# Optimization experiments

Measured on AMD Instinct MI355X. Metric: run time of the kernel, lower is better.

The kernel has to match this reference:

```python
import jax
jax.config.update("jax_enable_x64", True)
import jax.numpy as jnp
import numpy as np

SCALE = 1 << 16  # 65536 fixed-point scale
HALF = SCALE // 2

DIM = 4096
HIDDEN = 11008  # multiple_of * ceil(int(2*16384/3)/256)
TOKENS = 1024


def setup_inputs() -> dict:
    key = jax.random.key(0)
    kx, k1, k2, k3 = jax.random.split(key, 4)
    # Integer-valued fixed-point activations (torch code treats x as int32).
    x = jax.random.randint(kx, (TOKENS, DIM), 0, 256, dtype=jnp.int32)
    # Learned float weights (quantized to int32 fixed-point inside forward).
    w1 = jax.random.normal(k1, (HIDDEN, DIM), dtype=jnp.float32) * 0.02
    w2 = jax.random.normal(k2, (DIM, HIDDEN), dtype=jnp.float32) * 0.02
    w3 = jax.random.normal(k3, (HIDDEN, DIM), dtype=jnp.float32) * 0.02
    return {"x": x, "w1": w1, "w2": w2, "w3": w3}


def reference(x, w1, w2, w3):
    # Quantize weights to int32 fixed point (round half-to-even, like torch.round).
    w1i = jnp.round(w1.astype(jnp.float64) * SCALE).astype(jnp.int32)
    w2i = jnp.round(w2.astype(jnp.float64) * SCALE).astype(jnp.int32)
    w3i = jnp.round(w3.astype(jnp.float64) * SCALE).astype(jnp.int32)

    xf = x.astype(jnp.float64)  # [T, D]
    # Emulated integer GEMMs via fp64 matmul, truncated to int64 (exact here).
    t1 = jnp.matmul(xf, w1i.T.astype(jnp.float64)).astype(jnp.int64)  # [T, H]
    t3 = jnp.matmul(xf, w3i.T.astype(jnp.float64)).astype(jnp.int64)  # [T, H]

    # Requantize up-projection: rounding floor-div by SCALE (int floor division).
    q3 = ((t3 + HALF) // SCALE).astype(jnp.int32)

    # Gate path: requantize, dequantize to fp16, SiLU, re-quantize to int32.
    g = (t1 + HALF) // SCALE
    g = (g.astype(jnp.float64) / SCALE).astype(jnp.float16)
    g = jax.nn.silu(g)  # fp16 SiLU, matching F.silu on half
    g = jnp.round(g.astype(jnp.float64) * SCALE).astype(jnp.int32)

    # Fixed-point elementwise product with rounding requantization.
    t13 = ((g.astype(jnp.int64) * q3.astype(jnp.int64) + HALF) // SCALE).astype(jnp.int32)

    # Down projection GEMM + final requantization.
    t123 = jnp.matmul(t13.astype(jnp.float64), w2i.T.astype(jnp.float64)).astype(jnp.int64)
    out = ((t123 + HALF) // SCALE).astype(jnp.int32)  # [T, D]
    return out
```

## Files before the change

### kernel.cpp

```cpp
#include <hip/hip_runtime.h>
#include <hip/hip_fp16.h>
#include <math.h>

#define TOK  1024
#define DIMK 4096
#define HID  11008

typedef long long ll;
typedef int v4i  __attribute__((ext_vector_type(4)));
typedef int v16i __attribute__((ext_vector_type(16)));

#define T13_OFF 0ull
#define LUT_OFF 11272192ull
#define CS1_OFF (LUT_OFF + 32768ull)
#define CS3_OFF (CS1_OFF + 44032ull)
#define XQ_OFF  (CS3_OFF + 44032ull)
#define WQ_OFF  (XQ_OFF + 4194304ull)
#define PLANE   45088768ull
#define WS_NEED (WQ_OFF + 6ull * PLANE)

__device__ __forceinline__ int gate_requant(int g) {
  const float vf = __half2float(__float2half((float)g * (1.0f / 65536.0f)));
  const float e32 = (float)exp(-(double)vf);
  const float e16 = __half2float(__float2half(e32));
  const float d16 = __half2float(__float2half(1.0f + e16));
  const float s16 = __half2float(__float2half(1.0f / d16));
  const float p16 = __half2float(__float2half(vf * s16));
  return __float2int_rn(p16 * 65536.0f);
}

__device__ __forceinline__ v16i vzero16() {
  v16i z;
  #pragma unroll
  for (int i = 0; i < 16; ++i) z[i] = 0;
  return z;
}

__device__ __forceinline__ void gll(const void* g, void* l) {
  __builtin_amdgcn_global_load_lds((const __attribute__((address_space(1))) unsigned int*)g,
                                   (__attribute__((address_space(3))) unsigned int*)l,
                                   16, 0, 0);
}


__global__ void lut_kernel(int* __restrict__ lut) {
  const int i = blockIdx.x * blockDim.x + threadIdx.x;
  lut[i] = gate_requant(i - 4096);
}

__global__ __launch_bounds__(256)
void xq_kernel(const int* __restrict__ x, char* __restrict__ xq) {
  const size_t base = ((size_t)blockIdx.x * 256 + threadIdx.x) * 16;
  int w[4];
  #pragma unroll
  for (int i = 0; i < 4; ++i) {
    const int4 v = *reinterpret_cast<const int4*>(&x[base + i * 4]);
    w[i] = ((v.x & 255) | ((v.y & 255) << 8) | ((v.z & 255) << 16) | ((v.w & 255) << 24)) ^ 0x80808080;
  }
  *reinterpret_cast<int4*>(&xq[base]) = make_int4(w[0], w[1], w[2], w[3]);
}

__global__ __launch_bounds__(256)
void prequant_all(const float* __restrict__ w1, const float* __restrict__ w3,
                  const float* __restrict__ w2, char* __restrict__ wq,
                  int* __restrict__ cs1, int* __restrict__ cs3)
{
  const int bid = blockIdx.x;
  const int m = bid / 11008;
  const int rb = bid - m * 11008;
  const float* src = (m == 0) ? w1 : ((m == 1) ? w3 : w2);
  int4* lo = (int4*)(wq + (size_t)(2 * m) * PLANE);
  int4* hi = (int4*)(wq + (size_t)(2 * m + 1) * PLANE);
  const int t = threadIdx.x;
  const size_t fbase = (size_t)rb * 4096 + (size_t)t * 16;

  int sum = 0;
  int lob[4], hib[4];
  #pragma unroll
  for (int i = 0; i < 4; ++i) {
    const float4 f = *reinterpret_cast<const float4*>(&src[fbase + i * 4]);
    const int q0 = __float2int_rn(f.x * 65536.0f);
    const int q1 = __float2int_rn(f.y * 65536.0f);
    const int q2 = __float2int_rn(f.z * 65536.0f);
    const int q3 = __float2int_rn(f.w * 65536.0f);
    sum += q0 + q1 + q2 + q3;
    lob[i] = (q0 & 127) | ((q1 & 127) << 8) | ((q2 & 127) << 16) | ((q3 & 127) << 24);
    hib[i] = ((q0 >> 7) & 255) | (((q1 >> 7) & 255) << 8) |
             (((q2 >> 7) & 255) << 16) | (((q3 >> 7) & 255) << 24);
  }
  const size_t o = (size_t)rb * 256 + t;
  lo[o] = make_int4(lob[0], lob[1], lob[2], lob[3]);
  hi[o] = make_int4(hib[0], hib[1], hib[2], hib[3]);
  if (m < 2) {
    #pragma unroll
    for (int off = 32; off > 0; off >>= 1) sum += __shfl_xor(sum, off, 64);
    if ((t & 63) == 0) atomicAdd(((m == 0) ? cs1 : cs3) + rb, sum);
  }
}

#define UP_BUF 32768

__global__ __launch_bounds__(512, 1)
void up_gemm(const char* __restrict__ xq, const char* __restrict__ wq,
             const int* __restrict__ csum1, const int* __restrict__ csum3,
             const int* __restrict__ lut, char* __restrict__ t13)
{
  __shared__ char smem[3 * UP_BUF];
  const int tid = threadIdx.x;
  const int w = tid >> 6, l = tid & 63;
  const int rf = w & 3, cf = w >> 2;
  const int l16 = l * 16;

  const int flat = blockIdx.x;
  const int g = (flat & 7) * 86 + (flat >> 3);
  const int col0 = (g >> 2) * 64;
  const int row0 = (g & 3) * 256;

  const char* gA = xq + (size_t)(row0 + w * 32 + (l & 31)) * DIMK + (l >> 5) * 16;
  const char* gB = wq + (size_t)(w >> 1) * PLANE
                 + (size_t)(col0 + (w & 1) * 32 + (l & 31)) * DIMK + (l >> 5) * 16;
  const unsigned dA0 = (2 * w + 0) * 1024, dA1 = (2 * w + 1) * 1024;
  const unsigned dB0 = 16384 + (2 * w + 0) * 1024, dB1 = 16384 + (2 * w + 1) * 1024;

  v16i acc[2][4];
  #pragma unroll
  for (int m = 0; m < 2; ++m)
    #pragma unroll
    for (int p = 0; p < 4; ++p) acc[m][p] = vzero16();

  gll(gA, smem + dA0);       gll(gA + 32, smem + dA1);
  gll(gB, smem + dB0);       gll(gB + 32, smem + dB1);
  gll(gA + 64, smem + UP_BUF + dA0);  gll(gA + 96, smem + UP_BUF + dA1);
  gll(gB + 64, smem + UP_BUF + dB0);  gll(gB + 96, smem + UP_BUF + dB1);
  asm volatile("s_waitcnt vmcnt(4)" ::: "memory");
  __builtin_amdgcn_s_barrier();

  const int NT = DIMK / 64;
  unsigned co = 0, so = 2 * UP_BUF;
  for (int kt = 0; kt < NT; ++kt) {
    const char* sb = smem + co;
    const bool st = (kt + 2 < NT);
    const int kb = (kt + 2) * 64;
    {
      const v4i av0 = *(const v4i*)(sb + (rf * 4 + 0) * 1024 + l16);
      const v4i av1 = *(const v4i*)(sb + (rf * 4 + 2) * 1024 + l16);
      const v4i b0  = *(const v4i*)(sb + 16384 + (0 * 4 + cf * 2) * 1024 + l16);
      const v4i b1  = *(const v4i*)(sb + 16384 + (1 * 4 + cf * 2) * 1024 + l16);
      const v4i b2  = *(const v4i*)(sb + 16384 + (2 * 4 + cf * 2) * 1024 + l16);
      const v4i b3  = *(const v4i*)(sb + 16384 + (3 * 4 + cf * 2) * 1024 + l16);
      if (st) { gll(gA + kb, smem + so + dA0); gll(gA + kb + 32, smem + so + dA1); }
      __builtin_amdgcn_s_barrier();
      asm volatile("s_waitcnt lgkmcnt(0)" ::: "memory");
      __builtin_amdgcn_sched_barrier(0);
      __builtin_amdgcn_s_setprio(1);
      acc[0][0] = __builtin_amdgcn_mfma_i32_32x32x32_i8(av0, b0, acc[0][0], 0, 0, 0);
      acc[0][1] = __builtin_amdgcn_mfma_i32_32x32x32_i8(av0, b1, acc[0][1], 0, 0, 0);
      acc[0][2] = __builtin_amdgcn_mfma_i32_32x32x32_i8(av0, b2, acc[0][2], 0, 0, 0);
      acc[0][3] = __builtin_amdgcn_mfma_i32_32x32x32_i8(av0, b3, acc[0][3], 0, 0, 0);
      acc[1][0] = __builtin_amdgcn_mfma_i32_32x32x32_i8(av1, b0, acc[1][0], 0, 0, 0);
      acc[1][1] = __builtin_amdgcn_mfma_i32_32x32x32_i8(av1, b1, acc[1][1], 0, 0, 0);
      acc[1][2] = __builtin_amdgcn_mfma_i32_32x32x32_i8(av1, b2, acc[1][2], 0, 0, 0);
      acc[1][3] = __builtin_amdgcn_mfma_i32_32x32x32_i8(av1, b3, acc[1][3], 0, 0, 0);
      __builtin_amdgcn_s_setprio(0);
      __builtin_amdgcn_s_barrier();
    }
    {
      const v4i av0 = *(const v4i*)(sb + (rf * 4 + 1) * 1024 + l16);
      const v4i av1 = *(const v4i*)(sb + (rf * 4 + 3) * 1024 + l16);
      const v4i b0  = *(const v4i*)(sb + 16384 + (0 * 4 + cf * 2 + 1) * 1024 + l16);
      const v4i b1  = *(const v4i*)(sb + 16384 + (1 * 4 + cf * 2 + 1) * 1024 + l16);
      const v4i b2  = *(const v4i*)(sb + 16384 + (2 * 4 + cf * 2 + 1) * 1024 + l16);
      const v4i b3  = *(const v4i*)(sb + 16384 + (3 * 4 + cf * 2 + 1) * 1024 + l16);
      if (st) { gll(gB + kb, smem + so + dB0); gll(gB + kb + 32, smem + so + dB1); }
      __builtin_amdgcn_s_barrier();
      asm volatile("s_waitcnt lgkmcnt(0)" ::: "memory");
      __builtin_amdgcn_sched_barrier(0);
      __builtin_amdgcn_s_setprio(1);
      acc[0][0] = __builtin_amdgcn_mfma_i32_32x32x32_i8(av0, b0, acc[0][0], 0, 0, 0);
      acc[0][1] = __builtin_amdgcn_mfma_i32_32x32x32_i8(av0, b1, acc[0][1], 0, 0, 0);
      acc[0][2] = __builtin_amdgcn_mfma_i32_32x32x32_i8(av0, b2, acc[0][2], 0, 0, 0);
      acc[0][3] = __builtin_amdgcn_mfma_i32_32x32x32_i8(av0, b3, acc[0][3], 0, 0, 0);
      acc[1][0] = __builtin_amdgcn_mfma_i32_32x32x32_i8(av1, b0, acc[1][0], 0, 0, 0);
      acc[1][1] = __builtin_amdgcn_mfma_i32_32x32x32_i8(av1, b1, acc[1][1], 0, 0, 0);
      acc[1][2] = __builtin_amdgcn_mfma_i32_32x32x32_i8(av1, b2, acc[1][2], 0, 0, 0);
      acc[1][3] = __builtin_amdgcn_mfma_i32_32x32x32_i8(av1, b3, acc[1][3], 0, 0, 0);
      __builtin_amdgcn_s_setprio(0);
      if (st) { asm volatile("s_waitcnt vmcnt(4)" ::: "memory"); }
      else    { asm volatile("s_waitcnt vmcnt(0)" ::: "memory"); }
      __builtin_amdgcn_s_barrier();
    }
    if (st) so = (so == 2 * UP_BUF) ? 0 : so + UP_BUF;
    co = (co == 2 * UP_BUF) ? 0 : co + UP_BUF;
  }

  const int col = col0 + cf * 32 + (l & 31);
  const int cs1v = csum1[col], cs3v = csum3[col];
  #pragma unroll
  for (int m = 0; m < 2; ++m) {
    #pragma unroll
    for (int r = 0; r < 16; ++r) {
      const int row = row0 + rf * 64 + m * 32 + (r & 3) + 8 * (r >> 2) + 4 * (l >> 5);
      const ll t1 = (ll)acc[m][0][r] + (((ll)acc[m][1][r] + cs1v) << 7);
      int gg = (int)((t1 + 32768) >> 16);
      gg = gg < -4096 ? -4096 : (gg > 4095 ? 4095 : gg);
      const ll t3 = (ll)acc[m][2][r] + (((ll)acc[m][3][r] + cs3v) << 7);
      const int q3 = (int)((t3 + 32768) >> 16);
      const int gate = lut[gg + 4096];
      t13[(size_t)row * HID + col] = (char)((int)(((ll)gate * q3 + 32768) >> 16));
    }
  }
}

#define DN_BUF 24576

__global__ __launch_bounds__(512, 1)
void down_gemm(const char* __restrict__ t13, const char* __restrict__ w2lo,
               const char* __restrict__ w2hi, int* __restrict__ out)
{
  __shared__ char smem[3 * DN_BUF];
  const int tid = threadIdx.x;
  const int w = tid >> 6, l = tid & 63;
  const int rf = w & 3, cf = w >> 2;
  const int l16 = l * 16;

  const int flat = blockIdx.x;
  const int g = (flat & 7) * 32 + (flat >> 3);
  const int col0 = (g >> 2) * 64;
  const int row0 = (g & 3) * 256;

  const char* gA = t13 + (size_t)(row0 + w * 32 + (l & 31)) * HID + (l >> 5) * 16;
  const char* pB = (w >> 2) ? w2hi : w2lo;
  const char* gB = pB + (size_t)(col0 + ((w >> 1) & 1) * 32 + (l & 31)) * HID
                 + (w & 1) * 32 + (l >> 5) * 16;
  const unsigned dA0 = (2 * w + 0) * 1024, dA1 = (2 * w + 1) * 1024;
  const unsigned dB = 16384 + w * 1024;

  v16i acc[2][2];
  #pragma unroll
  for (int m = 0; m < 2; ++m)
    #pragma unroll
    for (int p = 0; p < 2; ++p) acc[m][p] = vzero16();

  gll(gA, smem + dA0);  gll(gA + 32, smem + dA1);  gll(gB, smem + dB);
  gll(gA + 64, smem + DN_BUF + dA0);  gll(gA + 96, smem + DN_BUF + dA1);
  gll(gB + 64, smem + DN_BUF + dB);
  asm volatile("s_waitcnt vmcnt(3)" ::: "memory");
  __builtin_amdgcn_s_barrier();

  const int NT = HID / 64;
  unsigned co = 0, so = 2 * DN_BUF;
  for (int kt = 0; kt < NT; ++kt) {
    const char* sb = smem + co;
    const bool st = (kt + 2 < NT);
    const int kb = (kt + 2) * 64;
    {
      const v4i av0 = *(const v4i*)(sb + (rf * 4 + 0) * 1024 + l16);
      const v4i av1 = *(const v4i*)(sb + (rf * 4 + 2) * 1024 + l16);
      const v4i bL  = *(const v4i*)(sb + 16384 + (0 * 4 + cf * 2) * 1024 + l16);
      const v4i bH  = *(const v4i*)(sb + 16384 + (1 * 4 + cf * 2) * 1024 + l16);
      if (st) { gll(gA + kb, smem + so + dA0); gll(gA + kb + 32, smem + so + dA1); }
      __builtin_amdgcn_s_barrier();
      asm volatile("s_waitcnt lgkmcnt(0)" ::: "memory");
      __builtin_amdgcn_sched_barrier(0);
      __builtin_amdgcn_s_setprio(1);
      acc[0][0] = __builtin_amdgcn_mfma_i32_32x32x32_i8(av0, bL, acc[0][0], 0, 0, 0);
      acc[0][1] = __builtin_amdgcn_mfma_i32_32x32x32_i8(av0, bH, acc[0][1], 0, 0, 0);
      acc[1][0] = __builtin_amdgcn_mfma_i32_32x32x32_i8(av1, bL, acc[1][0], 0, 0, 0);
      acc[1][1] = __builtin_amdgcn_mfma_i32_32x32x32_i8(av1, bH, acc[1][1], 0, 0, 0);
      __builtin_amdgcn_s_setprio(0);
      __builtin_amdgcn_s_barrier();
    }
    {
      const v4i av0 = *(const v4i*)(sb + (rf * 4 + 1) * 1024 + l16);
      const v4i av1 = *(const v4i*)(sb + (rf * 4 + 3) * 1024 + l16);
      const v4i bL  = *(const v4i*)(sb + 16384 + (0 * 4 + cf * 2 + 1) * 1024 + l16);
      const v4i bH  = *(const v4i*)(sb + 16384 + (1 * 4 + cf * 2 + 1) * 1024 + l16);
      if (st) { gll(gB + kb, smem + so + dB); }
      __builtin_amdgcn_s_barrier();
      asm volatile("s_waitcnt lgkmcnt(0)" ::: "memory");
      __builtin_amdgcn_sched_barrier(0);
      __builtin_amdgcn_s_setprio(1);
      acc[0][0] = __builtin_amdgcn_mfma_i32_32x32x32_i8(av0, bL, acc[0][0], 0, 0, 0);
      acc[0][1] = __builtin_amdgcn_mfma_i32_32x32x32_i8(av0, bH, acc[0][1], 0, 0, 0);
      acc[1][0] = __builtin_amdgcn_mfma_i32_32x32x32_i8(av1, bL, acc[1][0], 0, 0, 0);
      acc[1][1] = __builtin_amdgcn_mfma_i32_32x32x32_i8(av1, bH, acc[1][1], 0, 0, 0);
      __builtin_amdgcn_s_setprio(0);
      if (st) { asm volatile("s_waitcnt vmcnt(3)" ::: "memory"); }
      else    { asm volatile("s_waitcnt vmcnt(0)" ::: "memory"); }
      __builtin_amdgcn_s_barrier();
    }
    if (st) so = (so == 2 * DN_BUF) ? 0 : so + DN_BUF;
    co = (co == 2 * DN_BUF) ? 0 : co + DN_BUF;
  }

  const int col = col0 + cf * 32 + (l & 31);
  #pragma unroll
  for (int m = 0; m < 2; ++m) {
    #pragma unroll
    for (int r = 0; r < 16; ++r) {
      const int row = row0 + rf * 64 + m * 32 + (r & 3) + 8 * (r >> 2) + 4 * (l >> 5);
      out[(size_t)row * DIMK + col] =
          (int)((((ll)acc[m][0][r] + ((ll)acc[m][1][r] << 7)) + 32768) >> 16);
    }
  }
}

#define BT 64
#define BN 64
#define BK 64
#define LDST 68

__device__ __forceinline__ int mad24(int a, int b, int c) {
  return ((a << 8) >> 8) * ((b << 8) >> 8) + c;
}

__global__ __launch_bounds__(256)
void ffn_up_f(const int* __restrict__ x, const float* __restrict__ w1,
              const float* __restrict__ w3, short* __restrict__ t13)
{
  __shared__ int As[BT][LDST];
  __shared__ int B1[BK][LDST];
  __shared__ int B3[BK][LDST];
  const int tx = threadIdx.x, ty = threadIdx.y;
  const int tid = ty * 16 + tx;
  const int col0 = blockIdx.x * BN;
  const int row0 = blockIdx.y * BT;
  const int lr = tid >> 4;
  const int lk = (tid & 15) << 2;
  int acc1[16] = {0};
  int acc3[16] = {0};
  for (int k0 = 0; k0 < DIMK; k0 += BK) {
    #pragma unroll
    for (int m = 0; m < 4; ++m) {
      const int r = lr + m * 16;
      *reinterpret_cast<int4*>(&As[r][lk]) =
          *reinterpret_cast<const int4*>(&x[(size_t)(row0 + r) * DIMK + k0 + lk]);
      const float4 f1 = *reinterpret_cast<const float4*>(&w1[(size_t)(col0 + r) * DIMK + k0 + lk]);
      const float4 f3 = *reinterpret_cast<const float4*>(&w3[(size_t)(col0 + r) * DIMK + k0 + lk]);
      B1[lk + 0][r] = __float2int_rn(f1.x * 65536.0f);
      B1[lk + 1][r] = __float2int_rn(f1.y * 65536.0f);
      B1[lk + 2][r] = __float2int_rn(f1.z * 65536.0f);
      B1[lk + 3][r] = __float2int_rn(f1.w * 65536.0f);
      B3[lk + 0][r] = __float2int_rn(f3.x * 65536.0f);
      B3[lk + 1][r] = __float2int_rn(f3.y * 65536.0f);
      B3[lk + 2][r] = __float2int_rn(f3.z * 65536.0f);
      B3[lk + 3][r] = __float2int_rn(f3.w * 65536.0f);
    }
    __syncthreads();
    #pragma unroll 8
    for (int kk = 0; kk < BK; ++kk) {
      const int4 b1 = *reinterpret_cast<const int4*>(&B1[kk][tx << 2]);
      const int4 b3 = *reinterpret_cast<const int4*>(&B3[kk][tx << 2]);
      #pragma unroll
      for (int i = 0; i < 4; ++i) {
        const int av = As[(ty << 2) + i][kk] & 255;
        acc1[i*4+0] = mad24(av, b1.x, acc1[i*4+0]);
        acc1[i*4+1] = mad24(av, b1.y, acc1[i*4+1]);
        acc1[i*4+2] = mad24(av, b1.z, acc1[i*4+2]);
        acc1[i*4+3] = mad24(av, b1.w, acc1[i*4+3]);
        acc3[i*4+0] = mad24(av, b3.x, acc3[i*4+0]);
        acc3[i*4+1] = mad24(av, b3.y, acc3[i*4+1]);
        acc3[i*4+2] = mad24(av, b3.z, acc3[i*4+2]);
        acc3[i*4+3] = mad24(av, b3.w, acc3[i*4+3]);
      }
    }
    __syncthreads();
  }
  #pragma unroll
  for (int i = 0; i < 4; ++i) {
    #pragma unroll
    for (int j = 0; j < 4; ++j) {
      const int g    = (acc1[i*4+j] + 32768) >> 16;
      const int q3   = (acc3[i*4+j] + 32768) >> 16;
      const int gate = gate_requant(g);
      const int tv = (int)(((ll)gate * (ll)q3 + 32768) >> 16);
      t13[(size_t)(row0 + (ty<<2) + i) * HID + col0 + (tx<<2) + j] = (short)tv;
    }
  }
}

__global__ __launch_bounds__(256)
void ffn_down_f(const short* __restrict__ t13, const float* __restrict__ w2,
                int* __restrict__ out)
{
  __shared__ int As[BT][LDST];
  __shared__ int Bs[BK][LDST];
  const int tx = threadIdx.x, ty = threadIdx.y;
  const int tid = ty * 16 + tx;
  const int col0 = blockIdx.x * BN;
  const int row0 = blockIdx.y * BT;
  const int lr = tid >> 4;
  const int lk = (tid & 15) << 2;
  const int ar = tid >> 3;
  const int ak = (tid & 7) << 3;
  int acc[16] = {0};
  for (int k0 = 0; k0 < HID; k0 += BK) {
    #pragma unroll
    for (int m = 0; m < 2; ++m) {
      const int r = ar + m * 32;
      const int4 v = *reinterpret_cast<const int4*>(&t13[(size_t)(row0 + r) * HID + k0 + ak]);
      As[r][ak+0] = (v.x << 16) >> 16;  As[r][ak+1] = v.x >> 16;
      As[r][ak+2] = (v.y << 16) >> 16;  As[r][ak+3] = v.y >> 16;
      As[r][ak+4] = (v.z << 16) >> 16;  As[r][ak+5] = v.z >> 16;
      As[r][ak+6] = (v.w << 16) >> 16;  As[r][ak+7] = v.w >> 16;
    }
    #pragma unroll
    for (int m = 0; m < 4; ++m) {
      const int r = lr + m * 16;
      const float4 f = *reinterpret_cast<const float4*>(&w2[(size_t)(col0 + r) * HID + k0 + lk]);
      Bs[lk + 0][r] = __float2int_rn(f.x * 65536.0f);
      Bs[lk + 1][r] = __float2int_rn(f.y * 65536.0f);
      Bs[lk + 2][r] = __float2int_rn(f.z * 65536.0f);
      Bs[lk + 3][r] = __float2int_rn(f.w * 65536.0f);
    }
    __syncthreads();
    #pragma unroll 8
    for (int kk = 0; kk < BK; ++kk) {
      const int4 b = *reinterpret_cast<const int4*>(&Bs[kk][tx << 2]);
      #pragma unroll
      for (int i = 0; i < 4; ++i) {
        const int av = As[(ty << 2) + i][kk];
        acc[i*4+0] = mad24(av, b.x, acc[i*4+0]);
        acc[i*4+1] = mad24(av, b.y, acc[i*4+1]);
        acc[i*4+2] = mad24(av, b.z, acc[i*4+2]);
        acc[i*4+3] = mad24(av, b.w, acc[i*4+3]);
      }
    }
    __syncthreads();
  }
  #pragma unroll
  for (int i = 0; i < 4; ++i) {
    #pragma unroll
    for (int j = 0; j < 4; ++j) {
      out[(size_t)(row0 + (ty<<2) + i) * DIMK + col0 + (tx<<2) + j] =
          (acc[i*4+j] + 32768) >> 16;
    }
  }
}

extern "C" void kernel_launch(void* const* d_in, const int* in_sizes, int n_in,
                              void* d_out, int out_size, void* d_ws, size_t ws_size,
                              hipStream_t stream) {
  (void)in_sizes; (void)n_in; (void)out_size;
  const int*   x  = (const int*)d_in[0];
  const float* w1 = (const float*)d_in[1];
  const float* w2 = (const float*)d_in[2];
  const float* w3 = (const float*)d_in[3];
  int* out = (int*)d_out;
  char* ws = (char*)d_ws;

  if (ws_size >= WS_NEED) {
    char* t13 = ws + T13_OFF;
    int*  lut = (int*)(ws + LUT_OFF);
    int*  cs1 = (int*)(ws + CS1_OFF);
    int*  cs3 = (int*)(ws + CS3_OFF);
    char* xq  = ws + XQ_OFF;
    char* wq  = ws + WQ_OFF;

    hipMemsetAsync(ws + CS1_OFF, 0, 88064, stream);
    hipLaunchKernelGGL(lut_kernel, dim3(32), dim3(256), 0, stream, lut);
    hipLaunchKernelGGL(xq_kernel, dim3(1024), dim3(256), 0, stream, x, xq);
    hipLaunchKernelGGL(prequant_all, dim3(33024), dim3(256), 0, stream,
                       w1, w3, w2, wq, cs1, cs3);
    hipLaunchKernelGGL(up_gemm, dim3(688), dim3(512), 0, stream,
                       xq, wq, cs1, cs3, lut, t13);
    hipLaunchKernelGGL(down_gemm, dim3(256), dim3(512), 0, stream,
                       t13, wq + 4 * PLANE, wq + 5 * PLANE, out);
  } else {
    if (ws_size < (size_t)TOK * HID * sizeof(short)) return;
    short* t13 = (short*)ws;
    dim3 blk(16, 16);
    hipLaunchKernelGGL(ffn_up_f,   dim3(HID / BN, TOK / BT), blk, 0, stream, x, w1, w3, t13);
    hipLaunchKernelGGL(ffn_down_f, dim3(DIMK / BN, TOK / BT), blk, 0, stream, t13, w2, out);
  }
}
```

Measured before the change: 513.4 us.

## Replace LDS-staged up GEMM with direct global-to-register double-buffered loads

The up-projection GEMM no longer stages A and B tiles through a triple-buffered LDS ring with barriers. Each wave now loads its own MFMA operands straight from global memory into registers, double-buffered across k-steps, and launch bounds are raised to allow two blocks per CU. This removes LDS traffic and barrier synchronisation, but every wave now re-fetches data that was previously shared across waves. That multiplies global and L2 traffic for the shared A rows and B columns and raises register pressure.

```diff
diff --git a/kernel.cpp b/kernel.cpp
--- a/kernel.cpp
+++ b/kernel.cpp
@@ -98,29 +98,28 @@
   }
 }
 
-#define UP_BUF 32768
-
-__global__ __launch_bounds__(512, 1)
+
+__global__ __launch_bounds__(512, 2)
 void up_gemm(const char* __restrict__ xq, const char* __restrict__ wq,
              const int* __restrict__ csum1, const int* __restrict__ csum3,
              const int* __restrict__ lut, char* __restrict__ t13)
 {
-  __shared__ char smem[3 * UP_BUF];
   const int tid = threadIdx.x;
   const int w = tid >> 6, l = tid & 63;
   const int rf = w & 3, cf = w >> 2;
-  const int l16 = l * 16;
 
   const int flat = blockIdx.x;
   const int g = (flat & 7) * 86 + (flat >> 3);
   const int col0 = (g >> 2) * 64;
   const int row0 = (g & 3) * 256;
 
-  const char* gA = xq + (size_t)(row0 + w * 32 + (l & 31)) * DIMK + (l >> 5) * 16;
-  const char* gB = wq + (size_t)(w >> 1) * PLANE
-                 + (size_t)(col0 + (w & 1) * 32 + (l & 31)) * DIMK + (l >> 5) * 16;
-  const unsigned dA0 = (2 * w + 0) * 1024, dA1 = (2 * w + 1) * 1024;
-  const unsigned dB0 = 16384 + (2 * w + 0) * 1024, dB1 = 16384 + (2 * w + 1) * 1024;
+  const char* pa0 = xq + (size_t)(row0 + rf * 64 +  0 + (l & 31)) * DIMK + (l >> 5) * 16;
+  const char* pa1 = xq + (size_t)(row0 + rf * 64 + 32 + (l & 31)) * DIMK + (l >> 5) * 16;
+  const size_t offB = (size_t)(col0 + cf * 32 + (l & 31)) * DIMK + (l >> 5) * 16;
+  const char* pb0 = wq + 0ull * PLANE + offB;
+  const char* pb1 = wq + 1ull * PLANE + offB;
+  const char* pb2 = wq + 2ull * PLANE + offB;
+  const char* pb3 = wq + 3ull * PLANE + offB;
 
   v16i acc[2][4];
   #pragma unroll
@@ -128,70 +127,38 @@
     #pragma unroll
     for (int p = 0; p < 4; ++p) acc[m][p] = vzero16();
 
-  gll(gA, smem + dA0);       gll(gA + 32, smem + dA1);
-  gll(gB, smem + dB0);       gll(gB + 32, smem + dB1);
-  gll(gA + 64, smem + UP_BUF + dA0);  gll(gA + 96, smem + UP_BUF + dA1);
-  gll(gB + 64, smem + UP_BUF + dB0);  gll(gB + 96, smem + UP_BUF + dB1);
-  asm volatile("s_waitcnt vmcnt(4)" ::: "memory");
-  __builtin_amdgcn_s_barrier();
+  v4i a0[2][2], b0[4][2];
+  v4i a1[2][2], b1[4][2];
+
+  #define UP_LOAD(A, B, kb) { \
+    A[0][0] = *(const v4i*)(pa0 + (kb));      A[0][1] = *(const v4i*)(pa0 + (kb) + 32); \
+    A[1][0] = *(const v4i*)(pa1 + (kb));      A[1][1] = *(const v4i*)(pa1 + (kb) + 32); \
+    B[0][0] = *(const v4i*)(pb0 + (kb));      B[0][1] = *(const v4i*)(pb0 + (kb) + 32); \
+    B[1][0] = *(const v4i*)(pb1 + (kb));      B[1][1] = *(const v4i*)(pb1 + (kb) + 32); \
+    B[2][0] = *(const v4i*)(pb2 + (kb));      B[2][1] = *(const v4i*)(pb2 + (kb) + 32); \
+    B[3][0] = *(const v4i*)(pb3 + (kb));      B[3][1] = *(const v4i*)(pb3 + (kb) + 32); }
+
+  #define UP_MFMA(A, B) { \
+    _Pragma("unroll") \
+    for (int ks = 0; ks < 2; ++ks) { \
+      _Pragma("unroll") \
+      for (int m = 0; m < 2; ++m) { \
+        _Pragma("unroll") \
+        for (int p = 0; p < 4; ++p) { \
+          acc[m][p] = __builtin_amdgcn_mfma_i32_32x32x32_i8(A[m][ks], B[p][ks], acc[m][p], 0, 0, 0); \
+        } } } }
 
   const int NT = DIMK / 64;
-  unsigned co = 0, so = 2 * UP_BUF;
-  for (int kt = 0; kt < NT; ++kt) {
-    const char* sb = smem + co;
-    const bool st = (kt + 2 < NT);
-    const int kb = (kt + 2) * 64;
-    {
-      const v4i av0 = *(const v4i*)(sb + (rf * 4 + 0) * 1024 + l16);
-      const v4i av1 = *(const v4i*)(sb + (rf * 4 + 2) * 1024 + l16);
-      const v4i b0  = *(const v4i*)(sb + 16384 + (0 * 4 + cf * 2) * 1024 + l16);
-      const v4i b1  = *(const v4i*)(sb + 16384 + (1 * 4 + cf * 2) * 1024 + l16);
-      const v4i b2  = *(const v4i*)(sb + 16384 + (2 * 4 + cf * 2) * 1024 + l16);
-      const v4i b3  = *(const v4i*)(sb + 16384 + (3 * 4 + cf * 2) * 1024 + l16);
-      if (st) { gll(gA + kb, smem + so + dA0); gll(gA + kb + 32, smem + so + dA1); }
-      __builtin_amdgcn_s_barrier();
-      asm volatile("s_waitcnt lgkmcnt(0)" ::: "memory");
-      __builtin_amdgcn_sched_barrier(0);
-      __builtin_amdgcn_s_setprio(1);
-      acc[0][0] = __builtin_amdgcn_mfma_i32_32x32x32_i8(av0, b0, acc[0][0], 0, 0, 0);
-      acc[0][1] = __builtin_amdgcn_mfma_i32_32x32x32_i8(av0, b1, acc[0][1], 0, 0, 0);
-      acc[0][2] = __builtin_amdgcn_mfma_i32_32x32x32_i8(av0, b2, acc[0][2], 0, 0, 0);
-      acc[0][3] = __builtin_amdgcn_mfma_i32_32x32x32_i8(av0, b3, acc[0][3], 0, 0, 0);
-      acc[1][0] = __builtin_amdgcn_mfma_i32_32x32x32_i8(av1, b0, acc[1][0], 0, 0, 0);
-      acc[1][1] = __builtin_amdgcn_mfma_i32_32x32x32_i8(av1, b1, acc[1][1], 0, 0, 0);
-      acc[1][2] = __builtin_amdgcn_mfma_i32_32x32x32_i8(av1, b2, acc[1][2], 0, 0, 0);
-      acc[1][3] = __builtin_amdgcn_mfma_i32_32x32x32_i8(av1, b3, acc[1][3], 0, 0, 0);
-      __builtin_amdgcn_s_setprio(0);
-      __builtin_amdgcn_s_barrier();
-    }
-    {
-      const v4i av0 = *(const v4i*)(sb + (rf * 4 + 1) * 1024 + l16);
-      const v4i av1 = *(const v4i*)(sb + (rf * 4 + 3) * 1024 + l16);
-      const v4i b0  = *(const v4i*)(sb + 16384 + (0 * 4 + cf * 2 + 1) * 1024 + l16);
-      const v4i b1  = *(const v4i*)(sb + 16384 + (1 * 4 + cf * 2 + 1) * 1024 + l16);
-      const v4i b2  = *(const v4i*)(sb + 16384 + (2 * 4 + cf * 2 + 1) * 1024 + l16);
-      const v4i b3  = *(const v4i*)(sb + 16384 + (3 * 4 + cf * 2 + 1) * 1024 + l16);
-      if (st) { gll(gB + kb, smem + so + dB0); gll(gB + kb + 32, smem + so + dB1); }
-      __builtin_amdgcn_s_barrier();
-      asm volatile("s_waitcnt lgkmcnt(0)" ::: "memory");
-      __builtin_amdgcn_sched_barrier(0);
-      __builtin_amdgcn_s_setprio(1);
-      acc[0][0] = __builtin_amdgcn_mfma_i32_32x32x32_i8(av0, b0, acc[0][0], 0, 0, 0);
-      acc[0][1] = __builtin_amdgcn_mfma_i32_32x32x32_i8(av0, b1, acc[0][1], 0, 0, 0);
-      acc[0][2] = __builtin_amdgcn_mfma_i32_32x32x32_i8(av0, b2, acc[0][2], 0, 0, 0);
-      acc[0][3] = __builtin_amdgcn_mfma_i32_32x32x32_i8(av0, b3, acc[0][3], 0, 0, 0);
-      acc[1][0] = __builtin_amdgcn_mfma_i32_32x32x32_i8(av1, b0, acc[1][0], 0, 0, 0);
-      acc[1][1] = __builtin_amdgcn_mfma_i32_32x32x32_i8(av1, b1, acc[1][1], 0, 0, 0);
-      acc[1][2] = __builtin_amdgcn_mfma_i32_32x32x32_i8(av1, b2, acc[1][2], 0, 0, 0);
-      acc[1][3] = __builtin_amdgcn_mfma_i32_32x32x32_i8(av1, b3, acc[1][3], 0, 0, 0);
-      __builtin_amdgcn_s_setprio(0);
-      if (st) { asm volatile("s_waitcnt vmcnt(4)" ::: "memory"); }
-      else    { asm volatile("s_waitcnt vmcnt(0)" ::: "memory"); }
-      __builtin_amdgcn_s_barrier();
-    }
-    if (st) so = (so == 2 * UP_BUF) ? 0 : so + UP_BUF;
-    co = (co == 2 * UP_BUF) ? 0 : co + UP_BUF;
-  }
+  UP_LOAD(a0, b0, 0)
+  #pragma unroll 1
+  for (int kt = 0; kt < NT; kt += 2) {
+    UP_LOAD(a1, b1, (kt + 1) * 64)
+    UP_MFMA(a0, b0)
+    if (kt + 2 < NT) { UP_LOAD(a0, b0, (kt + 2) * 64) }
+    UP_MFMA(a1, b1)
+  }
+  #undef UP_LOAD
+  #undef UP_MFMA
 
   const int col = col0 + cf * 32 + (l & 31);
   const int cs1v = csum1[col], cs3v = csum3[col];
```

Result: slower. 842.7 us (+64.1%).

## Overlap w2 prequantization with up-projection GEMM via interleaved worker blocks

Applied to the files above, without the earlier changes.

The w2 quantization is taken out of the standalone prequant kernel and folded into the up-projection GEMM launch. Every fifth block quantizes 64 rows of w2 instead of doing GEMM work, and the remaining blocks are remapped to the original tile indices. The intent is to hide the memory-bound w2 conversion behind the compute-bound GEMM rather than running it serially. The risk is that these quantizer blocks occupy CUs and add memory traffic that competes with GEMM tiles, and the grid tail may change.

```diff
diff --git a/kernel.cpp b/kernel.cpp
--- a/kernel.cpp
+++ b/kernel.cpp
@@ -61,14 +61,13 @@
 }
 
 __global__ __launch_bounds__(256)
-void prequant_all(const float* __restrict__ w1, const float* __restrict__ w3,
-                  const float* __restrict__ w2, char* __restrict__ wq,
-                  int* __restrict__ cs1, int* __restrict__ cs3)
+void prequant13(const float* __restrict__ w1, const float* __restrict__ w3,
+                char* __restrict__ wq, int* __restrict__ cs1, int* __restrict__ cs3)
 {
   const int bid = blockIdx.x;
   const int m = bid / 11008;
   const int rb = bid - m * 11008;
-  const float* src = (m == 0) ? w1 : ((m == 1) ? w3 : w2);
+  const float* src = (m == 0) ? w1 : w3;
   int4* lo = (int4*)(wq + (size_t)(2 * m) * PLANE);
   int4* hi = (int4*)(wq + (size_t)(2 * m + 1) * PLANE);
   const int t = threadIdx.x;
@@ -91,11 +90,9 @@
   const size_t o = (size_t)rb * 256 + t;
   lo[o] = make_int4(lob[0], lob[1], lob[2], lob[3]);
   hi[o] = make_int4(hib[0], hib[1], hib[2], hib[3]);
-  if (m < 2) {
-    #pragma unroll
-    for (int off = 32; off > 0; off >>= 1) sum += __shfl_xor(sum, off, 64);
-    if ((t & 63) == 0) atomicAdd(((m == 0) ? cs1 : cs3) + rb, sum);
-  }
+  #pragma unroll
+  for (int off = 32; off > 0; off >>= 1) sum += __shfl_xor(sum, off, 64);
+  if ((t & 63) == 0) atomicAdd(((m == 0) ? cs1 : cs3) + rb, sum);
 }
 
 #define UP_BUF 32768
@@ -103,15 +100,45 @@
 __global__ __launch_bounds__(512, 1)
 void up_gemm(const char* __restrict__ xq, const char* __restrict__ wq,
              const int* __restrict__ csum1, const int* __restrict__ csum3,
-             const int* __restrict__ lut, char* __restrict__ t13)
+             const int* __restrict__ lut, char* __restrict__ t13,
+             const float* __restrict__ w2)
 {
   __shared__ char smem[3 * UP_BUF];
   const int tid = threadIdx.x;
+
+  if ((blockIdx.x % 5) == 4) {
+    const int qb = blockIdx.x / 5;
+    int4* lo = (int4*)(wq + 4ull * PLANE);
+    int4* hi = (int4*)(wq + 5ull * PLANE);
+    const int tt = tid & 255;
+    #pragma unroll 1
+    for (int cc = 0; cc < 32; ++cc) {
+      const int rb = qb * 64 + cc * 2 + (tid >> 8);
+      const size_t fbase = (size_t)rb * 4096 + (size_t)tt * 16;
+      int lob[4], hib[4];
+      #pragma unroll
+      for (int i = 0; i < 4; ++i) {
+        const float4 f = *reinterpret_cast<const float4*>(&w2[fbase + i * 4]);
+        const int q0 = __float2int_rn(f.x * 65536.0f);
+        const int q1 = __float2int_rn(f.y * 65536.0f);
+        const int q2 = __float2int_rn(f.z * 65536.0f);
+        const int q3 = __float2int_rn(f.w * 65536.0f);
+        lob[i] = (q0 & 127) | ((q1 & 127) << 8) | ((q2 & 127) << 16) | ((q3 & 127) << 24);
+        hib[i] = ((q0 >> 7) & 255) | (((q1 >> 7) & 255) << 8) |
+                 (((q2 >> 7) & 255) << 16) | (((q3 >> 7) & 255) << 24);
+      }
+      const size_t o = (size_t)rb * 256 + tt;
+      lo[o] = make_int4(lob[0], lob[1], lob[2], lob[3]);
+      hi[o] = make_int4(hib[0], hib[1], hib[2], hib[3]);
+    }
+    return;
+  }
+
   const int w = tid >> 6, l = tid & 63;
   const int rf = w & 3, cf = w >> 2;
   const int l16 = l * 16;
 
-  const int flat = blockIdx.x;
+  const int flat = (blockIdx.x / 5) * 4 + (blockIdx.x % 5);
   const int g = (flat & 7) * 86 + (flat >> 3);
   const int col0 = (g >> 2) * 64;
   const int row0 = (g & 3) * 256;
@@ -460,10 +487,10 @@
     hipMemsetAsync(ws + CS1_OFF, 0, 88064, stream);
     hipLaunchKernelGGL(lut_kernel, dim3(32), dim3(256), 0, stream, lut);
     hipLaunchKernelGGL(xq_kernel, dim3(1024), dim3(256), 0, stream, x, xq);
-    hipLaunchKernelGGL(prequant_all, dim3(33024), dim3(256), 0, stream,
-                       w1, w3, w2, wq, cs1, cs3);
-    hipLaunchKernelGGL(up_gemm, dim3(688), dim3(512), 0, stream,
-                       xq, wq, cs1, cs3, lut, t13);
+    hipLaunchKernelGGL(prequant13, dim3(22016), dim3(256), 0, stream,
+                       w1, w3, wq, cs1, cs3);
+    hipLaunchKernelGGL(up_gemm, dim3(860), dim3(512), 0, stream,
+                       xq, wq, cs1, cs3, lut, t13, w2);
     hipLaunchKernelGGL(down_gemm, dim3(256), dim3(512), 0, stream,
                        t13, wq + 4 * PLANE, wq + 5 * PLANE, out);
   } else {
```

Result: no change. 515.9 us (+0.5%).
